# Performance work log

Hardware: AMD Instinct MI355X
Metric: run time of the kernel (lower is better)

Reference implementation:

```python
import jax, jax.numpy as jnp
import numpy as np
from jax import lax

K = 8            # number of object slots
H = 250          # hidden / fc_size
EPS = 1e-5
DN = ('NCHW', 'OIHW', 'NCHW')


def ln_all(x):
    # F.layer_norm over all non-batch dims, no affine params (torch init: w=1,b=0)
    ax = tuple(range(1, x.ndim))
    m = jnp.mean(x, ax, keepdims=True)
    v = jnp.var(x, ax, keepdims=True)
    return (x - m) * lax.rsqrt(v + EPS)


def ln_last(x):
    # nn.LayerNorm(feat) -> last dim only
    m = jnp.mean(x, -1, keepdims=True)
    v = jnp.var(x, -1, keepdims=True)
    return (x - m) * lax.rsqrt(v + EPS)


def conv(x, w, b):
    # torch Conv2d(k=4, s=2, p=1), NCHW
    y = lax.conv_general_dilated(x, w, (2, 2), [(1, 1), (1, 1)], dimension_numbers=DN)
    return y + b[None, :, None, None]


def up4(x):
    return jnp.repeat(jnp.repeat(x, 4, axis=2), 4, axis=3)


def setup_inputs():
    ks = jax.random.split(jax.random.key(0), 20)
    bk = 48 * K
    p = lambda i, shape, s: jax.random.normal(ks[i], shape, jnp.float32) * s
    z = lambda n: jnp.zeros((n,), jnp.float32)
    return dict(
        x=p(0, (bk, 4096), 1.0),
        state=p(1, (bk, H), 1.0),
        # encoder convs (OIHW) + fc
        c1w=p(2, (16, 1, 4, 4), 0.25), c1b=z(16),
        c2w=p(3, (32, 16, 4, 4), 0.06), c2b=z(32),
        c3w=p(4, (64, 32, 4, 4), 0.04), c3b=z(64),
        efc_w=p(5, (4096, 512), 0.016), efc_b=z(512),
        # R_NEM (weights stored as [in, out])
        renc_w=p(6, (H, H), 0.06), renc_b=z(H),
        core_w=p(7, (2 * H, H), 0.045), core_b=z(H),
        ctx_w=p(8, (H, H), 0.06), ctx_b=z(H),
        att1_w=p(9, (H, 100), 0.06), att1_b=z(100),
        att2_w=p(10, (100, 1), 0.1), att2_b=z(1),
        out_w=p(11, (2 * H + 512, H), 0.03), out_b=z(H),
        # decoder fcs + convs
        dfc1_w=p(12, (H, 512), 0.06), dfc1_b=z(512),
        dfc2_w=p(13, (512, 4096), 0.045), dfc2_b=z(4096),
        d1w=p(14, (32, 64, 4, 4), 0.03), d1b=z(32),
        d2w=p(15, (16, 32, 4, 4), 0.045), d2b=z(16),
        d3w=p(16, (1, 16, 4, 4), 0.06), d3b=z(1),
    )


def reference(x, state, c1w, c1b, c2w, c2b, c3w, c3b, efc_w, efc_b,
              renc_w, renc_b, core_w, core_b, ctx_w, ctx_b,
              att1_w, att1_b, att2_w, att2_b, out_w, out_b,
              dfc1_w, dfc1_b, dfc2_w, dfc2_b, d1w, d1b, d2w, d2b, d3w, d3b):
    bk = x.shape[0]
    b = bk // K

    # ---------------- EncoderLayer ----------------
    def inwrap(h, w, bias):  # InputWrapper conv branch: NHWC -> permute(0,3,2,1) -> conv -> back
        y = conv(jnp.transpose(h, (0, 3, 2, 1)), w, bias)
        return jax.nn.elu(ln_all(jnp.transpose(y, (0, 3, 2, 1))))

    h = x.reshape(bk, 64, 64, 1)
    h = inwrap(h, c1w, c1b)                 # (bk,32,32,16)
    h = inwrap(h, c2w, c2b)                 # (bk,16,16,32)
    h = inwrap(h, c3w, c3b)                 # (bk,8,8,64)
    h = h.reshape(bk, -1)                   # (bk,4096)
    h = jax.nn.elu(ln_last(h @ efc_w + efc_b))   # (bk,512)

    # ---------------- R_NEM (RecurrentLayer) ----------------
    s1 = jax.nn.relu(ln_last(state @ renc_w + renc_b))   # (bk,H)
    s1r = s1.reshape(b, K, H)
    idx = np.array([[j for j in range(K) if j != i] for i in range(K)])  # (K,K-1)
    cs = s1r[:, idx, :]                                    # context: (b,K,K-1,H)
    fs = jnp.broadcast_to(s1r[:, :, None, :], cs.shape)    # focus copies
    pair = jnp.concatenate([fs, cs], axis=-1)              # (b,K,K-1,2H)
    core = jax.nn.relu(ln_last(pair @ core_w + core_b))    # (b,K,K-1,H)
    ctx = jax.nn.relu(ln_last(core @ ctx_w + ctx_b))       # (b,K,K-1,H)
    att = jax.nn.sigmoid(jnp.tanh(ln_last(core @ att1_w + att1_b)) @ att2_w + att2_b)  # (b,K,K-1,1)
    effect = jnp.sum(ctx * att, axis=2).reshape(bk, H)     # attention-weighted sum over K-1
    total = jnp.concatenate([s1, effect, h], axis=1)       # (bk, 2H+512)
    new_state = total @ out_w + out_b                      # (bk,H)
    xr = jax.nn.sigmoid(ln_last(new_state))
    state_out = jax.nn.sigmoid(new_state)

    # ---------------- DecoderLayer ----------------
    d = jax.nn.relu(ln_last(xr @ dfc1_w + dfc1_b))         # (bk,512)
    d = jax.nn.relu(ln_last(d @ dfc2_w + dfc2_b))          # (bk,4096)
    d = d.reshape(bk, 8, 8, 64)

    def outwrap(t, w, bias):
        y = conv(up4(jnp.transpose(t, (0, 3, 2, 1))), w, bias)
        return jnp.transpose(y, (0, 3, 2, 1))

    d = jax.nn.relu(ln_all(outwrap(d, d1w, d1b)))          # (bk,16,16,32)
    d = jax.nn.relu(ln_all(outwrap(d, d2w, d2b)))          # (bk,32,32,16)
    d = jax.nn.sigmoid(outwrap(d, d3w, d3b))               # (bk,64,64,1), no LN
    x_out = d.reshape(bk, -1)                              # (bk,4096)
    return x_out, state_out
```

## Files before the change

kernel.cpp:

```cpp
#include <hip/hip_runtime.h>
#include <hip/hip_bf16.h>
#include <math.h>

typedef __attribute__((ext_vector_type(8))) short bf16x8;
typedef __attribute__((ext_vector_type(4))) float f32x4;

__device__ __forceinline__ float eluf(float v){ return v > 0.f ? v : expm1f(v); }
__device__ __forceinline__ float sigf(float v){ return 1.f/(1.f+expf(-v)); }
__device__ __forceinline__ unsigned short f2bf(float f){
  unsigned u = __float_as_uint(f);
  u += 0x7FFFu + ((u >> 16) & 1u);
  return (unsigned short)(u >> 16);
}
__device__ __forceinline__ float bf2f(short s){
  return __uint_as_float(((unsigned)(unsigned short)s) << 16);
}

__device__ __forceinline__ void block_reduce2(float& a, float& b, float* sbuf){
  __syncthreads();
  for (int off = 32; off; off >>= 1){
    a += __shfl_down(a, off);
    b += __shfl_down(b, off);
  }
  int lane = threadIdx.x & 63, w = threadIdx.x >> 6;
  if (lane == 0){ sbuf[2*w] = a; sbuf[2*w+1] = b; }
  __syncthreads();
  if (threadIdx.x == 0){
    int nw = blockDim.x >> 6;
    float sa = 0.f, sb = 0.f;
    for (int i = 0; i < nw; i++){ sa += sbuf[2*i]; sb += sbuf[2*i+1]; }
    sbuf[0] = sa; sbuf[1] = sb;
  }
  __syncthreads();
  a = sbuf[0]; b = sbuf[1];
}

__device__ __forceinline__ float fold_sum(const float* __restrict__ w, int O, int I,
                                          int o, int i, int pa, int pb, int da, int db){
  float s = 0.f;
  for (int kh = 0; kh < 4; kh++){
    bool inh = (pb==0) ? (db==0 ? (kh==0) : (kh>=1)) : (db==0 ? (kh<=2) : (kh==3));
    if (!inh) continue;
    for (int kw = 0; kw < 4; kw++){
      bool inw = (pa==0) ? (da==0 ? (kw==0) : (kw>=1)) : (da==0 ? (kw<=2) : (kw==3));
      if (!inw) continue;
      s += w[((o*I + i)*4 + kh)*4 + kw];
    }
  }
  return s;
}
__device__ __forceinline__ void fold_elem(const float* __restrict__ w, float* __restrict__ CW,
                                          int O, int I, int l){
  int o = l % O; int q = l / O;
  int da = q & 1, db = (q>>1)&1, pa = (q>>2)&1, pb = (q>>3)&1, i = q>>4;
  CW[(((pb*2+pa)*4 + db*2+da)*I + i)*O + o] = fold_sum(w, O, I, o, i, pa, pb, da, db);
}
__device__ __forceinline__ void cvtc2_elem(const float* __restrict__ w, short* __restrict__ D, int l){
  int i = l & 15, t = (l>>4) & 15, o = l>>8;
  D[l] = (short)f2bf(w[(o*16 + i)*16 + t]);
}
__device__ __forceinline__ void cvtc3_elem(const float* __restrict__ w, short* __restrict__ D, int l){
  int i = l & 31, t = (l>>5) & 15, o = l>>9;
  D[l] = (short)f2bf(w[(o*32 + i)*16 + t]);
}
__device__ __forceinline__ void foldd1_elem(const float* __restrict__ w, short* __restrict__ D, int l){
  int i = l & 63, tap = (l>>6)&3, o = (l>>8)&31, ph = l>>13;
  D[l] = (short)f2bf(fold_sum(w, 32, 64, o, i, ph&1, ph>>1, tap&1, tap>>1));
}
__device__ __forceinline__ void foldd2_elem(const float* __restrict__ w, short* __restrict__ D, int l){
  int i = l & 31, tap = (l>>5)&3, o = (l>>7)&15, ph = l>>11;
  D[l] = (short)f2bf(fold_sum(w, 16, 32, o, i, ph&1, ph>>1, tap&1, tap>>1));
}

__global__ __launch_bounds__(256) void prep_combined(
  const float* __restrict__ efc,  short* __restrict__ Defc,
  const float* __restrict__ dfc2, short* __restrict__ Ddfc2,
  const float* __restrict__ outw, short* __restrict__ Dout,
  const float* __restrict__ corew,short* __restrict__ Dcore,
  const float* __restrict__ dfc1, short* __restrict__ Ddfc1,
  const float* __restrict__ renc, short* __restrict__ Drenc,
  const float* __restrict__ ctx,  const float* __restrict__ att1,
  short* __restrict__ Dctxatt,
  const float* __restrict__ d3w, float* __restrict__ CWT3,
  const float* __restrict__ c2w, short* __restrict__ BtC2,
  const float* __restrict__ c3w, short* __restrict__ BtC3,
  const float* __restrict__ d1w, short* __restrict__ BD1,
  const float* __restrict__ d2w, short* __restrict__ BD2,
  const float* __restrict__ state, short* __restrict__ SBF,
  short* __restrict__ TOTb)
{
  int bx = blockIdx.x;
  if (bx >= 1192){
    const int F3=256, P2=F3+8192, P3=P2+32768, P4=P3+32768, P5=P4+8192,
              ST=P5+98304, TP=ST+4608, TOTAL=TP+8704;
    for (int l = (bx-1192)*256 + threadIdx.x; l < TOTAL; l += 256*256){
      if (l < F3)      fold_elem(d3w, CWT3, 1, 16, l);
      else if (l < P2) cvtc2_elem(c2w, BtC2, l - F3);
      else if (l < P3) cvtc3_elem(c3w, BtC3, l - P2);
      else if (l < P4) foldd1_elem(d1w, BD1, l - P3);
      else if (l < P5) foldd2_elem(d2w, BD2, l - P4);
      else if (l < ST){
        int q = l - P5;
        int n = q >> 8, k = q & 255;
        SBF[q] = (k < 250) ? (short)f2bf(state[n*250 + k]) : (short)0;
      } else if (l < TP){
        int q = l - ST;
        int row = q / 12, cc = q % 12;
        int col = cc < 6 ? 250 + cc : 506 + (cc - 6);
        TOTb[row*1024 + col] = 0;
      } else {
        int q = l - TP;
        int r = q >> 8, cc = q & 255;
        int row = r < 6 ? 250 + r : 356 + (r - 6);
        Dctxatt[row*256 + cc] = 0;
      }
    }
    return;
  }
  const float* W; short* D; int K, N, Kp, base, mode = 0;
  if      (bx < 512) { W=efc;  D=Defc;  K=4096; N=512;  Kp=4096; base=0;    }
  else if (bx < 1024){ W=dfc2; D=Ddfc2; K=512;  N=4096; Kp=512;  base=512;  }
  else if (bx < 1088){ W=outw; D=Dout;  K=1012; N=250;  Kp=1024; base=1024; mode=2; }
  else if (bx < 1120){ W=corew;D=Dcore; K=500;  N=250;  Kp=512;  base=1088; mode=1; }
  else if (bx < 1152){ W=dfc1; D=Ddfc1; K=250;  N=512;  Kp=256;  base=1120; }
  else if (bx < 1168){ W=renc; D=Drenc; K=250;  N=250;  Kp=256;  base=1152; }
  else if (bx < 1184){ W=ctx;  D=Dctxatt;         K=250; N=250; Kp=256; base=1168; }
  else               { W=att1; D=Dctxatt + 65536; K=250; N=100; Kp=256; base=1184; }
  int t = bx - base;
  int tpr = Kp >> 6;
  int tk = t % tpr, tn = t / tpr;
  __shared__ short tile[64][65];
  int c = threadIdx.x & 63, r4 = threadIdx.x >> 6;
  int n0 = tn*64, k0 = tk*64;
  #pragma unroll 4
  for (int p = 0; p < 16; p++){
    int r = r4*16 + p;
    int k = k0 + r, n = n0 + c;
    int ksrc = k; bool valid;
    if (mode == 0) valid = (k < K);
    else if (mode == 1){ valid = (k < 250) || (k >= 256 && k < 506); ksrc = k < 256 ? k : k - 6; }
    else { valid = (k < 250) || (k >= 256 && k < 506) || (k >= 512);
           ksrc = k < 256 ? k : (k < 512 ? k - 6 : k - 12); }
    float v = (valid && n < N) ? W[(size_t)ksrc*N + n] : 0.f;
    tile[c][r] = (short)f2bf(v);
  }
  __syncthreads();
  #pragma unroll 4
  for (int p = 0; p < 16; p++){
    int nn = r4*16 + p;
    int n = n0 + nn;
    if (n < N) D[(size_t)n*Kp + k0 + c] = tile[nn][c];
  }
}

__device__ __forceinline__ void gemm_body(
    const short* __restrict__ Ab, const short* __restrict__ Bt,
    float* __restrict__ P, int M, int N, int Kp, int Kc,
    int bxx, int byy, int bzz)
{
  __shared__ __align__(16) short As[64*32];
  __shared__ __align__(16) short Bs[64*32];
  int tid = threadIdx.x;
  int bm = byy*64, bn = bxx*64;
  int kb = bzz * Kc;
  int kend = kb + Kc;

  int r = tid >> 2, c = tid & 3;
  const short* Arow = Ab + (size_t)(bm + r)*Kp;
  int gn = bn + r;
  bool bval = gn < N;
  const short* Brow = Bt + (size_t)gn*Kp;

  uint4 hA, hB;
  auto load_regs = [&](int k0){
    hA = *(const uint4*)&Arow[k0 + c*8];
    hB = bval ? *(const uint4*)&Brow[k0 + c*8] : make_uint4(0,0,0,0);
  };
  auto write_lds = [&](){
    *(uint4*)&As[r*32 + c*8] = hA;
    *(uint4*)&Bs[r*32 + c*8] = hB;
  };

  int wave = tid >> 6;
  int ln = tid & 15, quad = (tid >> 4) & 3;
  int wr = (wave >> 1) * 32, wc = (wave & 1) * 32;

  f32x4 zero = {0.f, 0.f, 0.f, 0.f};
  f32x4 acc[2][2] = {{zero, zero}, {zero, zero}};

  load_regs(kb);
  write_lds();
  __syncthreads();
  for (int k0 = kb; k0 < kend; k0 += 32){
    int nxt = k0 + 32;
    if (nxt < kend) load_regs(nxt);
    bf16x8 a0 = *(const bf16x8*)&As[(wr +      ln)*32 + quad*8];
    bf16x8 a1 = *(const bf16x8*)&As[(wr + 16 + ln)*32 + quad*8];
    bf16x8 b0 = *(const bf16x8*)&Bs[(wc +      ln)*32 + quad*8];
    bf16x8 b1 = *(const bf16x8*)&Bs[(wc + 16 + ln)*32 + quad*8];
    acc[0][0] = __builtin_amdgcn_mfma_f32_16x16x32_bf16(a0, b0, acc[0][0], 0, 0, 0);
    acc[0][1] = __builtin_amdgcn_mfma_f32_16x16x32_bf16(a0, b1, acc[0][1], 0, 0, 0);
    acc[1][0] = __builtin_amdgcn_mfma_f32_16x16x32_bf16(a1, b0, acc[1][0], 0, 0, 0);
    acc[1][1] = __builtin_amdgcn_mfma_f32_16x16x32_bf16(a1, b1, acc[1][1], 0, 0, 0);
    __syncthreads();
    if (nxt < kend){ write_lds(); __syncthreads(); }
  }

  float* Pout = P + (size_t)bzz*M*N;
  #pragma unroll
  for (int t = 0; t < 2; t++)
    #pragma unroll
    for (int u = 0; u < 2; u++)
      #pragma unroll
      for (int j = 0; j < 4; j++){
        int row = bm + wr + t*16 + quad*4 + j;
        int col = bn + wc + u*16 + ln;
        if (col < N) Pout[(size_t)row*N + col] = acc[t][u][j];
      }
}

__global__ __launch_bounds__(256) void gemm_mfma(
    const short* __restrict__ Ab, const short* __restrict__ Bt,
    float* __restrict__ P, int M, int N, int Kp, int Kc)
{
  gemm_body(Ab, Bt, P, M, N, Kp, Kc, blockIdx.x, blockIdx.y, blockIdx.z);
}

__device__ __forceinline__ void conv2g_body(
    const short* __restrict__ In, const short* __restrict__ Bt,
    short* __restrict__ Out, int bxx)
{
  __shared__ __align__(16) short As[128*32];
  __shared__ __align__(16) short Bs[32*32];
  int tid = threadIdx.x;
  int bm = bxx*128;

  int ra = tid >> 1, ca = (tid & 1)*16;
  int gr = bm + ra;
  int n = gr >> 8, pos = gr & 255;
  int oa = pos >> 4, ob = pos & 15;
  const short* ibase = In + (size_t)n*16384;
  int rb = tid >> 2, cb = (tid & 3)*8;
  const short* Brow = Bt + rb*256;
  bool bact = tid < 128;

  uint4 hA0, hA1, hB;
  auto load_regs = [&](int k0){
    #pragma unroll
    for (int h = 0; h < 2; h++){
      int k = k0 + ca + h*8;
      int tap = k >> 4;
      int ai = 2*oa + (tap & 3) - 1, bi = 2*ob + (tap >> 2) - 1;
      bool v = ((unsigned)ai < 32u) && ((unsigned)bi < 32u);
      uint4 tv = v ? *(const uint4*)&ibase[ai*512 + bi*16 + (k & 15)] : make_uint4(0,0,0,0);
      if (h == 0) hA0 = tv; else hA1 = tv;
    }
    if (bact) hB = *(const uint4*)&Brow[k0 + cb];
  };
  auto write_lds = [&](){
    *(uint4*)&As[ra*32 + ca] = hA0;
    *(uint4*)&As[ra*32 + ca + 8] = hA1;
    if (bact) *(uint4*)&Bs[rb*32 + cb] = hB;
  };

  int wave = tid >> 6, ln = tid & 15, quad = (tid >> 4) & 3;
  int wr = wave * 32;

  f32x4 zero = {0.f,0.f,0.f,0.f};
  f32x4 acc[2][2] = {{zero,zero},{zero,zero}};
  load_regs(0); write_lds(); __syncthreads();
  for (int k0 = 0; k0 < 256; k0 += 32){
    int nxt = k0 + 32;
    if (nxt < 256) load_regs(nxt);
    bf16x8 a0 = *(const bf16x8*)&As[(wr +      ln)*32 + quad*8];
    bf16x8 a1 = *(const bf16x8*)&As[(wr + 16 + ln)*32 + quad*8];
    bf16x8 b0 = *(const bf16x8*)&Bs[(     ln)*32 + quad*8];
    bf16x8 b1 = *(const bf16x8*)&Bs[(16 + ln)*32 + quad*8];
    acc[0][0] = __builtin_amdgcn_mfma_f32_16x16x32_bf16(a0, b0, acc[0][0], 0, 0, 0);
    acc[0][1] = __builtin_amdgcn_mfma_f32_16x16x32_bf16(a0, b1, acc[0][1], 0, 0, 0);
    acc[1][0] = __builtin_amdgcn_mfma_f32_16x16x32_bf16(a1, b0, acc[1][0], 0, 0, 0);
    acc[1][1] = __builtin_amdgcn_mfma_f32_16x16x32_bf16(a1, b1, acc[1][1], 0, 0, 0);
    __syncthreads();
    if (nxt < 256){ write_lds(); __syncthreads(); }
  }
  #pragma unroll
  for (int t = 0; t < 2; t++)
    #pragma unroll
    for (int u = 0; u < 2; u++)
      #pragma unroll
      for (int j = 0; j < 4; j++){
        int row = bm + wr + t*16 + quad*4 + j;
        int col = u*16 + ln;
        Out[(size_t)row*32 + col] = (short)f2bf(acc[t][u][j]);
      }
}

__device__ __forceinline__ void conv3_full_body(
    const short* __restrict__ E2raw, const float* __restrict__ bias2,
    const short* __restrict__ Bt3, const float* __restrict__ bias3,
    short* __restrict__ outp, int n)
{
  __shared__ __align__(16) short lsamp[18*18*40];
  __shared__ float sbuf[16];
  int tid = threadIdx.x;
  const short* ip = E2raw + (size_t)n*8192;
  float vv[32];
  float s = 0.f, s2 = 0.f;
  #pragma unroll
  for (int t = 0; t < 4; t++){
    bf16x8 v8 = *(const bf16x8*)&ip[(t*256 + tid)*8];
    #pragma unroll
    for (int j = 0; j < 8; j++){
      int e = (t*256 + tid)*8 + j;
      float v = bf2f(v8[j]) + bias2[e & 31];
      vv[t*8+j] = v; s += v; s2 += v*v;
    }
  }
  block_reduce2(s, s2, sbuf);
  float m2 = s*(1.f/8192.f);
  float rs2 = rsqrtf(s2*(1.f/8192.f) - m2*m2 + 1e-5f);
  for (int l = tid; l < 18*18*40/4; l += 256) ((unsigned long long*)lsamp)[l] = 0ull;
  __syncthreads();
  #pragma unroll
  for (int t = 0; t < 4; t++){
    int e0 = (t*256 + tid)*8;
    int slot = e0 >> 5, ch0 = e0 & 31;
    int a = slot >> 4, b = slot & 15;
    bf16x8 o8;
    #pragma unroll
    for (int j = 0; j < 8; j++)
      o8[j] = (short)f2bf(eluf((vv[t*8+j]-m2)*rs2));
    *(bf16x8*)&lsamp[((a+1)*18 + (b+1))*40 + ch0] = o8;
  }
  int wave = tid>>6, ln = tid&15, quad = (tid>>4)&3;
  int o3 = wave*16 + ln;
  bf16x8 bfr3[16];
  {
    const short* Brow = Bt3 + o3*512;
    #pragma unroll
    for (int ks = 0; ks < 16; ks++)
      bfr3[ks] = *(const bf16x8*)&Brow[ks*32 + quad*8];
  }
  __syncthreads();
  f32x4 z = {0.f,0.f,0.f,0.f};
  f32x4 acc3[4] = {z,z,z,z};
  #pragma unroll
  for (int ks = 0; ks < 16; ks++){
    int kh = ks>>2, kw = ks&3;
    #pragma unroll
    for (int mt = 0; mt < 4; mt++){
      int p = mt*16 + ln;
      int oa = p>>3, ob = p&7;
      bf16x8 a = *(const bf16x8*)&lsamp[((2*oa+kw)*18 + (2*ob+kh))*40 + quad*8];
      acc3[mt] = __builtin_amdgcn_mfma_f32_16x16x32_bf16(a, bfr3[ks], acc3[mt],0,0,0);
    }
  }
  s = 0.f; s2 = 0.f;
  float bz3 = bias3[o3];
  #pragma unroll
  for (int mt = 0; mt < 4; mt++)
    #pragma unroll
    for (int j = 0; j < 4; j++){
      float v = acc3[mt][j] + bz3;
      acc3[mt][j] = v; s += v; s2 += v*v;
    }
  block_reduce2(s, s2, sbuf);
  float m3 = s*(1.f/4096.f);
  float rs3 = rsqrtf(s2*(1.f/4096.f) - m3*m3 + 1e-5f);
  short* op = outp + (size_t)n*4096;
  #pragma unroll
  for (int mt = 0; mt < 4; mt++)
    #pragma unroll
    for (int j = 0; j < 4; j++){
      int p = mt*16 + quad*4 + j;
      int oa = p>>3, ob = p&7;
      op[oa*512 + ob*64 + o3] = f2bf(eluf((acc3[mt][j]-m3)*rs3));
    }
}

__device__ __forceinline__ void gemm_core_body(
    const short* __restrict__ Tb, const short* __restrict__ Bt,
    float* __restrict__ P, int M, int N, int Kc,
    int bxx, int byy, int bzz)
{
  __shared__ __align__(16) short As[64*32];
  __shared__ __align__(16) short Bs[64*32];
  int tid = threadIdx.x;
  int bm = byy*64, bn = bxx*64;
  int kb = bzz * Kc;
  int kend = kb + Kc;

  int r = tid >> 2, c = tid & 3;
  int gr = bm + r;
  int jj2 = gr % 7, fi2 = gr / 7;
  int ii = fi2 & 7, j2 = fi2 >> 3;
  int jidx = jj2 < ii ? jj2 : jj2 + 1;
  const short* own = Tb + (size_t)fi2*1024;
  const short* oth = Tb + (size_t)(j2*8 + jidx)*1024;
  int gn = bn + r;
  bool bval = gn < N;
  const short* Brow = Bt + (size_t)gn*512;

  uint4 hA, hB;
  auto load_regs = [&](int k0){
    int kk = k0 + c*8;
    const short* src = (kk & 256) ? oth : own;
    hA = *(const uint4*)&src[kk & 255];
    hB = bval ? *(const uint4*)&Brow[kk] : make_uint4(0,0,0,0);
  };
  auto write_lds = [&](){
    *(uint4*)&As[r*32 + c*8] = hA;
    *(uint4*)&Bs[r*32 + c*8] = hB;
  };

  int wave = tid >> 6;
  int ln = tid & 15, quad = (tid >> 4) & 3;
  int wr = (wave >> 1) * 32, wc = (wave & 1) * 32;

  f32x4 zero = {0.f, 0.f, 0.f, 0.f};
  f32x4 acc[2][2] = {{zero, zero}, {zero, zero}};

  load_regs(kb);
  write_lds();
  __syncthreads();
  for (int k0 = kb; k0 < kend; k0 += 32){
    int nxt = k0 + 32;
    if (nxt < kend) load_regs(nxt);
    bf16x8 a0 = *(const bf16x8*)&As[(wr +      ln)*32 + quad*8];
    bf16x8 a1 = *(const bf16x8*)&As[(wr + 16 + ln)*32 + quad*8];
    bf16x8 b0 = *(const bf16x8*)&Bs[(wc +      ln)*32 + quad*8];
    bf16x8 b1 = *(const bf16x8*)&Bs[(wc + 16 + ln)*32 + quad*8];
    acc[0][0] = __builtin_amdgcn_mfma_f32_16x16x32_bf16(a0, b0, acc[0][0], 0, 0, 0);
    acc[0][1] = __builtin_amdgcn_mfma_f32_16x16x32_bf16(a0, b1, acc[0][1], 0, 0, 0);
    acc[1][0] = __builtin_amdgcn_mfma_f32_16x16x32_bf16(a1, b0, acc[1][0], 0, 0, 0);
    acc[1][1] = __builtin_amdgcn_mfma_f32_16x16x32_bf16(a1, b1, acc[1][1], 0, 0, 0);
    __syncthreads();
    if (nxt < kend){ write_lds(); __syncthreads(); }
  }

  float* Pout = P + (size_t)bzz*M*N;
  #pragma unroll
  for (int t = 0; t < 2; t++)
    #pragma unroll
    for (int u = 0; u < 2; u++)
      #pragma unroll
      for (int j = 0; j < 4; j++){
        int row = bm + wr + t*16 + quad*4 + j;
        int col = bn + wc + u*16 + ln;
        if (col < N) Pout[(size_t)row*N + col] = acc[t][u][j];
      }
}

__device__ __forceinline__ void reduce_ln_body(
    const float* __restrict__ Pp, const float* __restrict__ bias,
    void* __restrict__ outp, int M, int N, int KS, int os, int act, int obf, int bmask,
    int row)
{
  __shared__ float rowbuf[4096];
  __shared__ float sbuf[16];
  size_t MN = (size_t)M*N;
  float s = 0.f, s2 = 0.f;
  for (int c = threadIdx.x; c < N; c += 256){
    float v = bias[c & bmask];
    for (int ks = 0; ks < KS; ks++) v += Pp[ks*MN + (size_t)row*N + c];
    rowbuf[c] = v; s += v; s2 += v*v;
  }
  block_reduce2(s, s2, sbuf);
  float m = s / N;
  float r = rsqrtf(s2/N - m*m + 1e-5f);
  for (int c = threadIdx.x; c < N; c += 256){
    float v = (rowbuf[c]-m)*r;
    if (act == 1) v = fmaxf(v, 0.f);
    else if (act == 2) v = eluf(v);
    else if (act == 3) v = tanhf(v);
    if (obf) ((short*)outp)[(size_t)row*os + c] = f2bf(v);
    else     ((float*)outp)[(size_t)row*os + c] = v;
  }
}

__global__ __launch_bounds__(256) void reduce_ln(
    const float* __restrict__ Pp, const float* __restrict__ bias,
    void* __restrict__ outp, int M, int N, int KS, int os, int act, int obf, int bmask)
{
  reduce_ln_body(Pp, bias, outp, M, N, KS, os, act, obf, bmask, blockIdx.x);
}

__device__ __forceinline__ void enc_conv1_body(
    const float* __restrict__ x, const float* __restrict__ w, const float* __restrict__ bias,
    short* __restrict__ outp, int n)
{
  __shared__ __align__(16) float in_t[66*68];
  __shared__ short rawb[16384];
  __shared__ float sbuf[16];
  int tid = threadIdx.x;
  for (int l = tid; l < 66*68; l += 256) in_t[l] = 0.f;
  __syncthreads();
  const float* xin = x + (size_t)n*4096;
  for (int l4 = tid; l4 < 1024; l4 += 256){
    float4 v = *(const float4*)&xin[l4*4];
    int aa = (l4*4) >> 6, bb = (l4*4) & 63;
    float* dst = &in_t[(aa+1)*68 + bb + 1];
    dst[0]=v.x; dst[1]=v.y; dst[2]=v.z; dst[3]=v.w;
  }
  int o = tid & 15;
  float wr[16];
  #pragma unroll
  for (int t = 0; t < 16; t++) wr[t] = w[o*16 + t];
  float bv = bias[o];
  __syncthreads();
  float s = 0.f, s2 = 0.f;
  for (int r = 0; r < 64; r++){
    int idx = tid + (r<<8);
    int bq = (idx>>4)&31, aq = idx>>9;
    int a0 = 2*aq, b0 = 2*bq;
    float acc = bv;
    #pragma unroll
    for (int kw = 0; kw < 4; kw++){
      const float* row = &in_t[(a0+kw)*68 + b0];
      float2 p0 = *(const float2*)&row[0];
      float2 p1 = *(const float2*)&row[2];
      acc += p0.x*wr[0*4+kw] + p0.y*wr[1*4+kw] + p1.x*wr[2*4+kw] + p1.y*wr[3*4+kw];
    }
    rawb[idx] = f2bf(acc);
    s += acc; s2 += acc*acc;
  }
  block_reduce2(s, s2, sbuf);
  float m = s*(1.f/16384.f);
  float rs = rsqrtf(s2*(1.f/16384.f) - m*m + 1e-5f);
  short* op = outp + (size_t)n*16384;
  for (int l = tid; l < 16384; l += 256){
    float v = bf2f(rawb[l]);
    op[l] = f2bf(eluf((v-m)*rs));
  }
}

__global__ __launch_bounds__(256) void fuse_a(
    const float* __restrict__ x, const float* __restrict__ c1w, const float* __restrict__ c1b,
    short* __restrict__ E1b,
    const short* __restrict__ SBF, const short* __restrict__ BT_renc, float* __restrict__ PB_renc)
{
  int b = blockIdx.x;
  if (b < 384){
    enc_conv1_body(x, c1w, c1b, E1b, b);
  } else {
    int id = b - 384;
    gemm_body(SBF, BT_renc, PB_renc, 384, 250, 256, 32, id & 3, (id >> 2) % 6, id / 24);
  }
}

__global__ __launch_bounds__(256) void fuse_b(
    const float* __restrict__ PB_renc, const float* __restrict__ renc_b, short* __restrict__ TOTb,
    const short* __restrict__ E1b, const short* __restrict__ BtC2, short* __restrict__ E2b)
{
  int b = blockIdx.x;
  if (b < 384){
    reduce_ln_body(PB_renc, renc_b, TOTb, 384, 250, 8, 1024, 1, 1, -1, b);
  } else {
    conv2g_body(E1b, BtC2, E2b, b - 384);
  }
}

__global__ __launch_bounds__(256) void fuse_c(
    const short* __restrict__ TOTb, const short* __restrict__ BT_core, float* __restrict__ PB_core,
    const short* __restrict__ E2b, const float* __restrict__ c2b,
    const short* __restrict__ BtC3, const float* __restrict__ c3b, short* __restrict__ E3b)
{
  int b = blockIdx.x;
  if (b < 336){
    gemm_core_body(TOTb, BT_core, PB_core, 2688, 250, 256, b % 4, (b / 4) % 42, b / 168);
  } else {
    conv3_full_body(E2b, c2b, BtC3, c3b, E3b, b - 336);
  }
}

__global__ __launch_bounds__(256) void fuse_d(
    const float* __restrict__ PB_core, const float* __restrict__ core_b, short* __restrict__ C1b,
    const short* __restrict__ E3b, const short* __restrict__ BT_efc, float* __restrict__ PB_efc)
{
  int b = blockIdx.x;
  if (b < 2688){
    reduce_ln_body(PB_core, core_b, C1b, 2688, 250, 2, 256, 1, 1, -1, b);
  } else {
    int id = b - 2688;
    gemm_body(E3b, BT_efc, PB_efc, 384, 512, 4096, 512, id & 7, (id >> 3) % 6, id / 48);
  }
}

__global__ __launch_bounds__(256) void fuse_e(
    const short* __restrict__ C1b, const short* __restrict__ BT_ctxatt, float* __restrict__ PB_ctxatt,
    const float* __restrict__ PB_efc, const float* __restrict__ efc_b, short* __restrict__ TOTh)
{
  int b = blockIdx.x;
  if (b < 504){
    gemm_body(C1b, BT_ctxatt, PB_ctxatt, 2688, 384, 256, 128, b % 6, (b / 6) % 42, b / 252);
  } else {
    reduce_ln_body(PB_efc, efc_b, TOTh, 384, 512, 8, 1024, 2, 1, -1, b - 504);
  }
}

__global__ __launch_bounds__(256) void reduce_ns(
    const float* __restrict__ Pp, const float* __restrict__ bias,
    short* __restrict__ XRb, float* __restrict__ so, int M, int N, int KS)
{
  __shared__ float rowbuf[256];
  __shared__ float sbuf[16];
  int row = blockIdx.x;
  size_t MN = (size_t)M*N;
  float s = 0.f, s2 = 0.f;
  for (int c = threadIdx.x; c < N; c += 256){
    float v = bias[c];
    for (int ks = 0; ks < KS; ks++) v += Pp[ks*MN + (size_t)row*N + c];
    rowbuf[c] = v; s += v; s2 += v*v;
  }
  block_reduce2(s, s2, sbuf);
  float m = s / N;
  float r = rsqrtf(s2/N - m*m + 1e-5f);
  for (int c = threadIdx.x; c < N; c += 256){
    float v = rowbuf[c];
    XRb[(size_t)row*256 + c] = f2bf(sigf((v-m)*r));
    so[(size_t)row*N + c] = sigf(v);
  }
}

__global__ __launch_bounds__(448) void ctx_att_effect(
    const float* __restrict__ Pc, const float* __restrict__ ctx_b,
    const float* __restrict__ att1_b,
    const float* __restrict__ w2, const float* __restrict__ b2,
    short* __restrict__ tot)
{
  __shared__ float ctxs[7][250];
  __shared__ float att_s[7];
  int fi = blockIdx.x, tid = threadIdx.x;
  int jj = tid >> 6, lane = tid & 63;
  const size_t MN = (size_t)2688*384;
  int row = fi*7 + jj;
  float vv[4];
  float s = 0.f, s2 = 0.f;
  #pragma unroll
  for (int t = 0; t < 4; t++){
    int c = lane + t*64;
    float v = 0.f;
    if (c < 250) v = ctx_b[c] + Pc[(size_t)row*384 + c] + Pc[MN + (size_t)row*384 + c];
    vv[t] = v; s += v; s2 += v*v;
  }
  #pragma unroll
  for (int off = 32; off; off >>= 1){ s += __shfl_down(s, off); s2 += __shfl_down(s2, off); }
  s = __shfl(s, 0); s2 = __shfl(s2, 0);
  float m = s*(1.f/250.f);
  float r = rsqrtf(s2*(1.f/250.f) - m*m + 1e-5f);
  #pragma unroll
  for (int t = 0; t < 4; t++){
    int c = lane + t*64;
    if (c < 250) ctxs[jj][c] = fmaxf((vv[t]-m)*r, 0.f);
  }
  float va[2];
  s = 0.f; s2 = 0.f;
  #pragma unroll
  for (int t = 0; t < 2; t++){
    int c = lane + t*64;
    float v = 0.f;
    if (c < 100)
      v = att1_b[c] + Pc[(size_t)row*384 + 256 + c] + Pc[MN + (size_t)row*384 + 256 + c];
    va[t] = v; s += v; s2 += v*v;
  }
  #pragma unroll
  for (int off = 32; off; off >>= 1){ s += __shfl_down(s, off); s2 += __shfl_down(s2, off); }
  s = __shfl(s, 0); s2 = __shfl(s2, 0);
  m = s*0.01f;
  r = rsqrtf(s2*0.01f - m*m + 1e-5f);
  float d = 0.f;
  #pragma unroll
  for (int t = 0; t < 2; t++){
    int c = lane + t*64;
    if (c < 100) d += tanhf((va[t]-m)*r)*w2[c];
  }
  #pragma unroll
  for (int off = 32; off; off >>= 1) d += __shfl_down(d, off);
  if (lane == 0) att_s[jj] = sigf(d + b2[0]);
  __syncthreads();
  for (int h = tid; h < 250; h += 448){
    float sum = 0.f;
    #pragma unroll
    for (int q = 0; q < 7; q++) sum += ctxs[q][h]*att_s[q];
    tot[(size_t)fi*1024 + 256 + h] = f2bf(sum);
  }
}

__global__ __launch_bounds__(256) void dec_conv12_mfma(
    const short* __restrict__ in, const short* __restrict__ Bd1, const float* __restrict__ bias1,
    const short* __restrict__ Bd2, const float* __restrict__ bias2, short* __restrict__ outp)
{
  __shared__ __align__(16) short smem[18*18*40];
  __shared__ float sbuf[16];
  int n = blockIdx.x, tid = threadIdx.x;
  for (int l = tid; l < 1800; l += 256) ((unsigned long long*)smem)[l] = 0ull;
  __syncthreads();
  const short* ip = in + (size_t)n*4096;
  for (int l = tid; l < 1024; l += 256){
    int i4 = l & 15, sb = (l>>4)&7, sa = l>>7;
    *(uint2*)&smem[((sa+1)*10 + (sb+1))*72 + i4*4] = *(const uint2*)&ip[sa*512 + sb*64 + i4*4];
  }
  int wave = tid>>6, ln = tid&15, quad = (tid>>4)&3;
  int pa = wave & 1, pb = wave >> 1;
  bf16x8 bfr1[2][8];
  #pragma unroll
  for (int nt = 0; nt < 2; nt++){
    const short* Brow = Bd1 + (wave*32 + nt*16 + ln)*256;
    #pragma unroll
    for (int ks = 0; ks < 8; ks++)
      bfr1[nt][ks] = *(const bf16x8*)&Brow[ks*32 + quad*8];
  }
  __syncthreads();
  f32x4 z = {0.f,0.f,0.f,0.f};
  f32x4 acc[2][4] = {{z,z,z,z},{z,z,z,z}};
  #pragma unroll
  for (int ks = 0; ks < 8; ks++){
    int tap = ks>>1, ibase = (ks&1)*32 + quad*8;
    int da = tap & 1, db = tap >> 1;
    #pragma unroll
    for (int mt = 0; mt < 4; mt++){
      int p = mt*16 + ln;
      int ta = p>>3, tb = p&7;
      bf16x8 a = *(const bf16x8*)&smem[((ta+da+pa)*10 + (tb+db+pb))*72 + ibase];
      acc[0][mt] = __builtin_amdgcn_mfma_f32_16x16x32_bf16(a, bfr1[0][ks], acc[0][mt],0,0,0);
      acc[1][mt] = __builtin_amdgcn_mfma_f32_16x16x32_bf16(a, bfr1[1][ks], acc[1][mt],0,0,0);
    }
  }
  float s = 0.f, s2 = 0.f;
  #pragma unroll
  for (int nt = 0; nt < 2; nt++){
    float bz = bias1[nt*16 + ln];
    #pragma unroll
    for (int mt = 0; mt < 4; mt++)
      #pragma unroll
      for (int j = 0; j < 4; j++){
        float v = acc[nt][mt][j] + bz;
        acc[nt][mt][j] = v; s += v; s2 += v*v;
      }
  }
  block_reduce2(s, s2, sbuf);
  float m1 = s*(1.f/8192.f);
  float rs1 = rsqrtf(s2*(1.f/8192.f) - m1*m1 + 1e-5f);
  bf16x8 bfr2[4];
  {
    const short* Brow = Bd2 + (wave*16 + ln)*128;
    #pragma unroll
    for (int ks = 0; ks < 4; ks++)
      bfr2[ks] = *(const bf16x8*)&Brow[ks*32 + quad*8];
  }
  for (int l = tid; l < 3240; l += 256) ((unsigned long long*)smem)[l] = 0ull;
  __syncthreads();
  #pragma unroll
  for (int nt = 0; nt < 2; nt++){
    int o = nt*16 + ln;
    #pragma unroll
    for (int mt = 0; mt < 4; mt++)
      #pragma unroll
      for (int j = 0; j < 4; j++){
        int p = mt*16 + quad*4 + j;
        int ta = p>>3, tb = p&7;
        int sa = 2*ta + pa, sb = 2*tb + pb;
        smem[((sa+1)*18 + (sb+1))*40 + o] = f2bf(fmaxf((acc[nt][mt][j]-m1)*rs1, 0.f));
      }
  }
  __syncthreads();
  f32x4 acc2[16] = {z,z,z,z,z,z,z,z,z,z,z,z,z,z,z,z};
  #pragma unroll
  for (int ks = 0; ks < 4; ks++){
    int da = ks & 1, db = ks >> 1;
    #pragma unroll
    for (int mt = 0; mt < 16; mt++){
      int p = mt*16 + ln;
      int ta = p>>4, tb = p&15;
      bf16x8 a = *(const bf16x8*)&smem[((ta+da+pa)*18 + (tb+db+pb))*40 + quad*8];
      acc2[mt] = __builtin_amdgcn_mfma_f32_16x16x32_bf16(a, bfr2[ks], acc2[mt],0,0,0);
    }
  }
  s = 0.f; s2 = 0.f;
  float bz2 = bias2[ln];
  #pragma unroll
  for (int mt = 0; mt < 16; mt++)
    #pragma unroll
    for (int j = 0; j < 4; j++){
      float v = acc2[mt][j] + bz2;
      acc2[mt][j] = v; s += v; s2 += v*v;
    }
  block_reduce2(s, s2, sbuf);
  float m = s*(1.f/16384.f);
  float rs = rsqrtf(s2*(1.f/16384.f) - m*m + 1e-5f);
  short* op = outp + (size_t)n*16384;
  #pragma unroll
  for (int mt = 0; mt < 16; mt++)
    #pragma unroll
    for (int j = 0; j < 4; j++){
      int p = mt*16 + quad*4 + j;
      int ta = p>>4, tb = p&15;
      op[(2*ta+pa)*512 + (2*tb+pb)*16 + ln] = f2bf(fmaxf((acc2[mt][j]-m)*rs, 0.f));
    }
}

__global__ __launch_bounds__(256) void dec_conv3_ig(
    const short* __restrict__ in, const float* __restrict__ CWT, const float* __restrict__ bias,
    float* __restrict__ outp)
{
  __shared__ __align__(16) float in_t[9792];
  __shared__ __align__(16) float wl[256];
  int bx = blockIdx.x;
  int n = bx >> 1, b0 = (bx & 1) * 32, tb0 = b0 >> 1;
  int tid = threadIdx.x;
  const short* ip = in + (size_t)n*16384;
  for (int l = tid; l < 9792; l += 256){
    int i = l & 15, sb = (l >> 4) % 18, sap = l / 288;
    int sa = sap - 1, sbg = tb0 - 1 + sb;
    float v = 0.f;
    if ((unsigned)sa < 32u && (unsigned)sbg < 32u)
      v = bf2f(ip[sa*512 + sbg*16 + i]);
    in_t[(sap*18 + sb)*16 + i] = v;
  }
  for (int l = tid; l < 256; l += 256) wl[l] = CWT[l];
  __syncthreads();
  float bv = bias[0];
  int bl = tid & 31, ath = tid >> 5;
  int b = b0 + bl;
  int tb = b >> 1, pb = b & 1;
  float* op = outp + (size_t)n*4096;
  #pragma unroll
  for (int j = 0; j < 8; j++){
    int a = ath*8 + j;
    int ta = a >> 1, pa = a & 1;
    float4 s4 = make_float4(0.f,0.f,0.f,0.f);
    #pragma unroll
    for (int db = 0; db < 2; db++){
      int sb = tb + db + (pb ? 0 : -1);
      int sbl = sb - (tb0 - 1);
      #pragma unroll
      for (int da = 0; da < 2; da++){
        int sa = ta + da + (pa ? 0 : -1);
        int sap = sa + 1;
        const float4* A4 = (const float4*)&in_t[(sap*18 + sbl)*16];
        const float4* B4 = (const float4*)&wl[((pb*2+pa)*4 + db*2+da)*16];
        #pragma unroll
        for (int q = 0; q < 4; q++){
          float4 av = A4[q], bw = B4[q];
          s4.x += av.x*bw.x; s4.y += av.y*bw.y;
          s4.z += av.z*bw.z; s4.w += av.w*bw.w;
        }
      }
    }
    op[a*64 + b] = sigf(bv + s4.x + s4.y + s4.z + s4.w);
  }
}

extern "C" void kernel_launch(void* const* d_in, const int* in_sizes, int n_in,
                              void* d_out, int out_size, void* d_ws, size_t ws_size,
                              hipStream_t stream) {
  const float* x      = (const float*)d_in[0];
  const float* state  = (const float*)d_in[1];
  const float* c1w    = (const float*)d_in[2];
  const float* c1b    = (const float*)d_in[3];
  const float* c2w    = (const float*)d_in[4];
  const float* c2b    = (const float*)d_in[5];
  const float* c3w    = (const float*)d_in[6];
  const float* c3b    = (const float*)d_in[7];
  const float* efc_w  = (const float*)d_in[8];
  const float* efc_b  = (const float*)d_in[9];
  const float* renc_w = (const float*)d_in[10];
  const float* renc_b = (const float*)d_in[11];
  const float* core_w = (const float*)d_in[12];
  const float* core_b = (const float*)d_in[13];
  const float* ctx_w  = (const float*)d_in[14];
  const float* ctx_b  = (const float*)d_in[15];
  const float* att1_w = (const float*)d_in[16];
  const float* att1_b = (const float*)d_in[17];
  const float* att2_w = (const float*)d_in[18];
  const float* att2_b = (const float*)d_in[19];
  const float* out_w  = (const float*)d_in[20];
  const float* out_b  = (const float*)d_in[21];
  const float* dfc1_w = (const float*)d_in[22];
  const float* dfc1_b = (const float*)d_in[23];
  const float* dfc2_w = (const float*)d_in[24];
  const float* dfc2_b = (const float*)d_in[25];
  const float* d1w    = (const float*)d_in[26];
  const float* d1b    = (const float*)d_in[27];
  const float* d2w    = (const float*)d_in[28];
  const float* d2b    = (const float*)d_in[29];
  const float* d3w    = (const float*)d_in[30];
  const float* d3b    = (const float*)d_in[31];

  float* wsf = (float*)d_ws;
  size_t o = 0;
  float* PB_renc   = wsf + o; o += (size_t)8*384*250;
  float* PB_core   = wsf + o; o += (size_t)2*2688*250;
  float* PB_efc    = wsf + o; o += (size_t)8*384*512;
  float* PB_ctxatt = wsf + o; o += (size_t)2*2688*384;
  float* PB_out    = wsf + o; o += (size_t)8*384*250;
  float* PB_dfc1   = wsf + o; o += (size_t)4*384*512;
  float* PB_dfc2   = wsf + o; o += (size_t)384*4096;
  float* CWT3 = wsf + o; o += 256;
  short* E1b  = (short*)(wsf + o); o += (size_t)384*16384/2;
  short* E2b  = (short*)(wsf + o); o += (size_t)384*8192/2;
  short* E3b  = (short*)(wsf + o); o += (size_t)384*4096/2;
  short* TOTb = (short*)(wsf + o); o += (size_t)384*1024/2;
  short* C1b  = (short*)(wsf + o); o += (size_t)2688*256/2;
  short* XRb  = (short*)(wsf + o); o += (size_t)384*256/2;
  short* G1b  = (short*)(wsf + o); o += (size_t)384*512/2;
  short* SBF  = (short*)(wsf + o); o += (size_t)384*256/2;
  short* BtC2 = (short*)(wsf + o); o += 8192/2;
  short* BtC3 = (short*)(wsf + o); o += 32768/2;
  short* BD1  = (short*)(wsf + o); o += 32768/2;
  short* BD2  = (short*)(wsf + o); o += 8192/2;
  short* BT_efc    = (short*)(wsf + o); o += 2097152/2;
  short* BT_renc   = (short*)(wsf + o); o += 64000/2;
  short* BT_core   = (short*)(wsf + o); o += 128000/2;
  short* BT_ctxatt = (short*)(wsf + o); o += 98304/2;
  short* BT_out    = (short*)(wsf + o); o += 256000/2;
  short* BT_dfc1   = (short*)(wsf + o); o += 131072/2;
  short* BT_dfc2   = (short*)(wsf + o); o += 2097152/2;
  short* D2b = E1b;
  short* G2b = E3b;

  float* xout = (float*)d_out;
  float* sout = xout + (size_t)384*4096;

  prep_combined<<<1448, 256, 0, stream>>>(
      efc_w, BT_efc, dfc2_w, BT_dfc2, out_w, BT_out, core_w, BT_core,
      dfc1_w, BT_dfc1, renc_w, BT_renc, ctx_w, att1_w, BT_ctxatt,
      d3w, CWT3, c2w, BtC2, c3w, BtC3, d1w, BD1, d2w, BD2, state, SBF, TOTb);

  fuse_a<<<576, 256, 0, stream>>>(x, c1w, c1b, E1b, SBF, BT_renc, PB_renc);
  fuse_b<<<1152, 256, 0, stream>>>(PB_renc, renc_b, TOTb, E1b, BtC2, E2b);
  fuse_c<<<720, 256, 0, stream>>>(TOTb, BT_core, PB_core, E2b, c2b, BtC3, c3b, E3b);
  fuse_d<<<3072, 256, 0, stream>>>(PB_core, core_b, C1b, E3b, BT_efc, PB_efc);
  fuse_e<<<888, 256, 0, stream>>>(C1b, BT_ctxatt, PB_ctxatt, PB_efc, efc_b, TOTb+512);

  ctx_att_effect<<<384, 448, 0, stream>>>(PB_ctxatt, ctx_b, att1_b, att2_w, att2_b, TOTb);

  gemm_mfma<<<dim3(4,6,8), 256, 0, stream>>>(TOTb, BT_out, PB_out, 384, 250, 1024, 128);
  reduce_ns<<<384, 256, 0, stream>>>(PB_out, out_b, XRb, sout, 384, 250, 8);

  gemm_mfma<<<dim3(8,6,4), 256, 0, stream>>>(XRb, BT_dfc1, PB_dfc1, 384, 512, 256, 64);
  reduce_ln<<<384, 256, 0, stream>>>(PB_dfc1, dfc1_b, G1b, 384, 512, 4, 512, 1, 1, -1);
  gemm_mfma<<<dim3(64,6,1), 256, 0, stream>>>(G1b, BT_dfc2, PB_dfc2, 384, 4096, 512, 512);
  reduce_ln<<<384, 256, 0, stream>>>(PB_dfc2, dfc2_b, G2b, 384, 4096, 1, 4096, 1, 1, -1);

  dec_conv12_mfma<<<384, 256, 0, stream>>>(G2b, BD1, d1b, BD2, d2b, D2b);
  dec_conv3_ig<<<768, 256, 0, stream>>>(D2b, CWT3, d3b, xout);

  (void)in_sizes; (void)n_in; (void)out_size; (void)ws_size;
}
```

Baseline: 293.7 us.

## Move big weight transposes into fuse_b and fuse dfc2 LayerNorm into decoder conv

The large efc and dfc2 weight transposes move out of the serial prep kernel and run as extra blocks inside fuse_b, alongside the conv2 and renc-reduce work. The dfc2 bias-add plus LayerNorm and ReLU is folded into the decoder conv12 kernel, which reads the fp32 GEMM output directly. This removes one launch and the bf16 intermediate round trip. The cost is a longer critical path in fuse_b and scalar, non-vectorised shared-memory stores in the decoder prologue.

```diff
diff --git a/kernel.cpp b/kernel.cpp
--- a/kernel.cpp
+++ b/kernel.cpp
@@ -73,8 +73,6 @@
 }
 
 __global__ __launch_bounds__(256) void prep_combined(
-  const float* __restrict__ efc,  short* __restrict__ Defc,
-  const float* __restrict__ dfc2, short* __restrict__ Ddfc2,
   const float* __restrict__ outw, short* __restrict__ Dout,
   const float* __restrict__ corew,short* __restrict__ Dcore,
   const float* __restrict__ dfc1, short* __restrict__ Ddfc1,
@@ -90,10 +88,10 @@
   short* __restrict__ TOTb)
 {
   int bx = blockIdx.x;
-  if (bx >= 1192){
+  if (bx >= 168){
     const int F3=256, P2=F3+8192, P3=P2+32768, P4=P3+32768, P5=P4+8192,
               ST=P5+98304, TP=ST+4608, TOTAL=TP+8704;
-    for (int l = (bx-1192)*256 + threadIdx.x; l < TOTAL; l += 256*256){
+    for (int l = (bx-168)*256 + threadIdx.x; l < TOTAL; l += 256*256){
       if (l < F3)      fold_elem(d3w, CWT3, 1, 16, l);
       else if (l < P2) cvtc2_elem(c2w, BtC2, l - F3);
       else if (l < P3) cvtc3_elem(c3w, BtC3, l - P2);
@@ -118,14 +116,12 @@
     return;
   }
   const float* W; short* D; int K, N, Kp, base, mode = 0;
-  if      (bx < 512) { W=efc;  D=Defc;  K=4096; N=512;  Kp=4096; base=0;    }
-  else if (bx < 1024){ W=dfc2; D=Ddfc2; K=512;  N=4096; Kp=512;  base=512;  }
-  else if (bx < 1088){ W=outw; D=Dout;  K=1012; N=250;  Kp=1024; base=1024; mode=2; }
-  else if (bx < 1120){ W=corew;D=Dcore; K=500;  N=250;  Kp=512;  base=1088; mode=1; }
-  else if (bx < 1152){ W=dfc1; D=Ddfc1; K=250;  N=512;  Kp=256;  base=1120; }
-  else if (bx < 1168){ W=renc; D=Drenc; K=250;  N=250;  Kp=256;  base=1152; }
-  else if (bx < 1184){ W=ctx;  D=Dctxatt;         K=250; N=250; Kp=256; base=1168; }
-  else               { W=att1; D=Dctxatt + 65536; K=250; N=100; Kp=256; base=1184; }
+  if      (bx < 64) { W=outw; D=Dout;  K=1012; N=250;  Kp=1024; base=0;   mode=2; }
+  else if (bx < 96) { W=corew;D=Dcore; K=500;  N=250;  Kp=512;  base=64;  mode=1; }
+  else if (bx < 128){ W=dfc1; D=Ddfc1; K=250;  N=512;  Kp=256;  base=96;  }
+  else if (bx < 144){ W=renc; D=Drenc; K=250;  N=250;  Kp=256;  base=128; }
+  else if (bx < 160){ W=ctx;  D=Dctxatt;         K=250; N=250; Kp=256; base=144; }
+  else              { W=att1; D=Dctxatt + 65536; K=250; N=100; Kp=256; base=160; }
   int t = bx - base;
   int tpr = Kp >> 6;
   int tk = t % tpr, tn = t / tpr;
@@ -153,6 +149,30 @@
   }
 }
 
+__device__ __forceinline__ void wtrans_body(
+    const float* __restrict__ W, short* __restrict__ D, int K, int N, int t)
+{
+  int tpr = K >> 6;
+  int tk = t % tpr, tn = t / tpr;
+  __shared__ short tile[64][65];
+  int c = threadIdx.x & 63, r4 = threadIdx.x >> 6;
+  int n0 = tn*64, k0 = tk*64;
+  #pragma unroll 4
+  for (int p = 0; p < 16; p++){
+    int r = r4*16 + p;
+    int k = k0 + r, n = n0 + c;
+    float v = (n < N) ? W[(size_t)k*N + n] : 0.f;
+    tile[c][r] = (short)f2bf(v);
+  }
+  __syncthreads();
+  #pragma unroll 4
+  for (int p = 0; p < 16; p++){
+    int nn = r4*16 + p;
+    int n = n0 + nn;
+    if (n < N) D[(size_t)n*K + k0 + c] = tile[nn][c];
+  }
+}
+
 __device__ __forceinline__ void gemm_body(
     const short* __restrict__ Ab, const short* __restrict__ Bt,
     float* __restrict__ P, int M, int N, int Kp, int Kc,
@@ -550,13 +570,19 @@
 
 __global__ __launch_bounds__(256) void fuse_b(
     const float* __restrict__ PB_renc, const float* __restrict__ renc_b, short* __restrict__ TOTb,
-    const short* __restrict__ E1b, const short* __restrict__ BtC2, short* __restrict__ E2b)
+    const short* __restrict__ E1b, const short* __restrict__ BtC2, short* __restrict__ E2b,
+    const float* __restrict__ efc_w, short* __restrict__ BT_efc,
+    const float* __restrict__ dfc2_w, short* __restrict__ BT_dfc2)
 {
   int b = blockIdx.x;
   if (b < 384){
     reduce_ln_body(PB_renc, renc_b, TOTb, 384, 250, 8, 1024, 1, 1, -1, b);
+  } else if (b < 1152){
+    conv2g_body(E1b, BtC2, E2b, b - 384);
   } else {
-    conv2g_body(E1b, BtC2, E2b, b - 384);
+    int id = b - 1152;
+    if (id < 512) wtrans_body(efc_w, BT_efc, 4096, 512, id);
+    else          wtrans_body(dfc2_w, BT_dfc2, 512, 4096, id - 512);
   }
 }
 
@@ -686,19 +712,33 @@
   }
 }
 
-__global__ __launch_bounds__(256) void dec_conv12_mfma(
-    const short* __restrict__ in, const short* __restrict__ Bd1, const float* __restrict__ bias1,
+__global__ __launch_bounds__(256) void dec_ln_conv12(
+    const float* __restrict__ Pp, const float* __restrict__ biasln,
+    const short* __restrict__ Bd1, const float* __restrict__ bias1,
     const short* __restrict__ Bd2, const float* __restrict__ bias2, short* __restrict__ outp)
 {
   __shared__ __align__(16) short smem[18*18*40];
   __shared__ float sbuf[16];
   int n = blockIdx.x, tid = threadIdx.x;
+  const float* Prow = Pp + (size_t)n*4096;
+  float vln[16];
+  float sl = 0.f, sl2 = 0.f;
+  #pragma unroll
+  for (int k = 0; k < 16; k++){
+    int c = k*256 + tid;
+    float v = biasln[c] + Prow[c];
+    vln[k] = v; sl += v; sl2 += v*v;
+  }
+  block_reduce2(sl, sl2, sbuf);
+  float ml = sl*(1.f/4096.f);
+  float rl = rsqrtf(sl2*(1.f/4096.f) - ml*ml + 1e-5f);
   for (int l = tid; l < 1800; l += 256) ((unsigned long long*)smem)[l] = 0ull;
   __syncthreads();
-  const short* ip = in + (size_t)n*4096;
-  for (int l = tid; l < 1024; l += 256){
-    int i4 = l & 15, sb = (l>>4)&7, sa = l>>7;
-    *(uint2*)&smem[((sa+1)*10 + (sb+1))*72 + i4*4] = *(const uint2*)&ip[sa*512 + sb*64 + i4*4];
+  #pragma unroll
+  for (int k = 0; k < 16; k++){
+    int c = k*256 + tid;
+    int sa = c >> 9, sb = (c >> 6) & 7, i = c & 63;
+    smem[((sa+1)*10 + (sb+1))*72 + i] = (short)f2bf(fmaxf((vln[k]-ml)*rl, 0.f));
   }
   int wave = tid>>6, ln = tid&15, quad = (tid>>4)&3;
   int pa = wave & 1, pb = wave >> 1;
@@ -917,18 +957,18 @@
   short* BT_dfc1   = (short*)(wsf + o); o += 131072/2;
   short* BT_dfc2   = (short*)(wsf + o); o += 2097152/2;
   short* D2b = E1b;
-  short* G2b = E3b;
 
   float* xout = (float*)d_out;
   float* sout = xout + (size_t)384*4096;
 
-  prep_combined<<<1448, 256, 0, stream>>>(
-      efc_w, BT_efc, dfc2_w, BT_dfc2, out_w, BT_out, core_w, BT_core,
-      dfc1_w, BT_dfc1, renc_w, BT_renc, ctx_w, att1_w, BT_ctxatt,
+  prep_combined<<<424, 256, 0, stream>>>(
+      out_w, BT_out, core_w, BT_core, dfc1_w, BT_dfc1, renc_w, BT_renc,
+      ctx_w, att1_w, BT_ctxatt,
       d3w, CWT3, c2w, BtC2, c3w, BtC3, d1w, BD1, d2w, BD2, state, SBF, TOTb);
 
   fuse_a<<<576, 256, 0, stream>>>(x, c1w, c1b, E1b, SBF, BT_renc, PB_renc);
-  fuse_b<<<1152, 256, 0, stream>>>(PB_renc, renc_b, TOTb, E1b, BtC2, E2b);
+  fuse_b<<<2176, 256, 0, stream>>>(PB_renc, renc_b, TOTb, E1b, BtC2, E2b,
+                                   efc_w, BT_efc, dfc2_w, BT_dfc2);
   fuse_c<<<720, 256, 0, stream>>>(TOTb, BT_core, PB_core, E2b, c2b, BtC3, c3b, E3b);
   fuse_d<<<3072, 256, 0, stream>>>(PB_core, core_b, C1b, E3b, BT_efc, PB_efc);
   fuse_e<<<888, 256, 0, stream>>>(C1b, BT_ctxatt, PB_ctxatt, PB_efc, efc_b, TOTb+512);
@@ -941,9 +981,8 @@
   gemm_mfma<<<dim3(8,6,4), 256, 0, stream>>>(XRb, BT_dfc1, PB_dfc1, 384, 512, 256, 64);
   reduce_ln<<<384, 256, 0, stream>>>(PB_dfc1, dfc1_b, G1b, 384, 512, 4, 512, 1, 1, -1);
   gemm_mfma<<<dim3(64,6,1), 256, 0, stream>>>(G1b, BT_dfc2, PB_dfc2, 384, 4096, 512, 512);
-  reduce_ln<<<384, 256, 0, stream>>>(PB_dfc2, dfc2_b, G2b, 384, 4096, 1, 4096, 1, 1, -1);
-
-  dec_conv12_mfma<<<384, 256, 0, stream>>>(G2b, BD1, d1b, BD2, d2b, D2b);
+
+  dec_ln_conv12<<<384, 256, 0, stream>>>(PB_dfc2, dfc2_b, BD1, d1b, BD2, d2b, D2b);
   dec_conv3_ig<<<768, 256, 0, stream>>>(D2b, CWT3, d3b, xout);
 
   (void)in_sizes; (void)n_in; (void)out_size; (void)ws_size;
```

After: 301.7 us, median of 2. 2.7% more time.
